# Optimization experiments

Measured on AMD Instinct MI355X. Metric: run time of the kernel, lower is better.

## Reference

```python
import jax, jax.numpy as jnp
from jax import lax
import numpy as np

B, T, I, H, O = 2048, 256, 88, 64, 13


def _lstm_layer(xs, w_ih, w_hh, b):
    # xs: [T, B, in], w_ih: [4H, in], w_hh: [4H, H], b: [4H] (b_ih + b_hh)
    Bb = xs.shape[1]
    Hh = w_hh.shape[1]

    def step(carry, x_t):
        h, c = carry
        g = x_t @ w_ih.T + h @ w_hh.T + b  # [B, 4H]
        i, f, gg, o = jnp.split(g, 4, axis=-1)  # PyTorch gate order: i, f, g, o
        i = jax.nn.sigmoid(i)
        f = jax.nn.sigmoid(f)
        gg = jnp.tanh(gg)
        o = jax.nn.sigmoid(o)
        c = f * c + i * gg
        h = o * jnp.tanh(c)
        return (h, c), h

    init = (jnp.zeros((Bb, Hh), xs.dtype), jnp.zeros((Bb, Hh), xs.dtype))
    (h_last, _), ys = lax.scan(step, init, xs)
    return ys, h_last


def setup_inputs() -> dict:
    key = jax.random.key(0)
    ks = jax.random.split(key, 12)
    s = lambda fan: 1.0 / np.sqrt(H)  # PyTorch LSTM init scale 1/sqrt(H)
    u = lambda k, shape: jax.random.uniform(k, shape, jnp.float32, -s(H), s(H))
    return {
        "x": jax.random.normal(ks[0], (B, T, I), jnp.float32),
        "w_ih0": u(ks[1], (4 * H, I)),
        "w_hh0": u(ks[2], (4 * H, H)),
        "b_ih0": u(ks[3], (4 * H,)),
        "b_hh0": u(ks[4], (4 * H,)),
        "w_ih1": u(ks[5], (4 * H, H)),
        "w_hh1": u(ks[6], (4 * H, H)),
        "b_ih1": u(ks[7], (4 * H,)),
        "b_hh1": u(ks[8], (4 * H,)),
        "fc_w": u(ks[9], (O, H)),
        "fc_b": u(ks[10], (O,)),
    }


def reference(x, w_ih0, w_hh0, b_ih0, b_hh0, w_ih1, w_hh1, b_ih1, b_hh1, fc_w, fc_b):
    xs = jnp.transpose(x, (1, 0, 2))  # [T, B, I]
    ys1, _ = _lstm_layer(xs, w_ih0, w_hh0, b_ih0 + b_hh0)  # [T, B, H]
    # inter-layer dropout and head dropout are identity in eval mode
    _, h_last = _lstm_layer(ys1, w_ih1, w_hh1, b_ih1 + b_hh1)  # [B, H]
    return h_last @ fc_w.T + fc_b  # [B, O]
```

## Files before the change

### kernel.cpp

```cpp
#include <hip/hip_runtime.h>
#include <hip/hip_bf16.h>


#define B_ 2048
#define T_ 256
#define I_ 88
#define H_ 64
#define O_ 13
#define NB 8
#define G4H 256

__device__ __align__(16) float g_ys1[(size_t)T_ * B_ * H_];
__device__ __align__(16) float g_wp[(I_ + H_ + H_ + H_) * G4H];

__device__ __forceinline__ float sigmoid_f(float v) {
    return 1.f / (1.f + __expf(-v));
}
__device__ __forceinline__ float tanh_f(float v) {
    return 1.f - 2.f / (__expf(2.f * v) + 1.f);
}

__global__ void prep_weights(const float* __restrict__ wih0, const float* __restrict__ whh0,
                             const float* __restrict__ wih1, const float* __restrict__ whh1) {
    int id = blockIdx.x * blockDim.x + threadIdx.x;
    const int S0 = I_ * G4H;
    const int S1 = S0 + H_ * G4H;
    const int S2 = S1 + H_ * G4H;
    const int S3 = S2 + H_ * G4H;
    if (id >= S3) return;
    const float* src;
    int base, K;
    if (id < S0)      { base = 0;  src = wih0; K = I_; }
    else if (id < S1) { base = S0; src = whh0; K = H_; }
    else if (id < S2) { base = S1; src = wih1; K = H_; }
    else              { base = S2; src = whh1; K = H_; }
    int loc = id - base;
    int k   = loc >> 8;
    int col = loc & 255;
    int hh  = col >> 2;
    int g   = col & 3;
    g_wp[id] = src[(g * H_ + hh) * K + k];
}

__global__ __launch_bounds__(256, 1) void lstm_l0(const float* __restrict__ x,
                                                  const float* __restrict__ bih,
                                                  const float* __restrict__ bhh) {
    extern __shared__ float sm[];
    float* w0  = sm;
    float* wh  = sm + I_ * G4H;
    float* hsh = sm + (I_ + H_) * G4H;

    const int tid = threadIdx.x;
    for (int i = tid; i < ((I_ + H_) * G4H) / 4; i += 256)
        ((float4*)sm)[i] = ((const float4*)g_wp)[i];
    for (int i = tid; i < NB * H_; i += 256) hsh[i] = 0.f;

    const int hh = tid & 63;
    const int rg = __builtin_amdgcn_readfirstlane(tid >> 6);
    const int row0 = blockIdx.x * NB + rg * 2;
    const float* xr0 = x + (size_t)row0 * (T_ * I_);
    const float* xr1 = xr0 + (T_ * I_);

    const float b0 = bih[hh] + bhh[hh];
    const float b1 = bih[64 + hh] + bhh[64 + hh];
    const float b2 = bih[128 + hh] + bhh[128 + hh];
    const float b3 = bih[192 + hh] + bhh[192 + hh];

    float c0 = 0.f, c1 = 0.f;
    float* ys0 = g_ys1 + (size_t)row0 * H_ + hh;

    __syncthreads();

    for (int t = 0; t < T_; ++t) {
        float a00 = b0, a01 = b1, a02 = b2, a03 = b3;
        float a10 = b0, a11 = b1, a12 = b2, a13 = b3;
        const float* xt0 = xr0 + t * I_;
        const float* xt1 = xr1 + t * I_;
#pragma unroll 8
        for (int k = 0; k < I_; ++k) {
            const float4 w = *(const float4*)&w0[(k << 8) + (hh << 2)];
            const float xv0 = xt0[k];
            const float xv1 = xt1[k];
            a00 += w.x * xv0; a01 += w.y * xv0; a02 += w.z * xv0; a03 += w.w * xv0;
            a10 += w.x * xv1; a11 += w.y * xv1; a12 += w.z * xv1; a13 += w.w * xv1;
        }
        const float* hc = hsh + (t & 1) * (NB * H_) + rg * 128;
#pragma unroll 8
        for (int k = 0; k < H_; ++k) {
            const float4 w = *(const float4*)&wh[(k << 8) + (hh << 2)];
            const float hv0 = hc[k];
            const float hv1 = hc[64 + k];
            a00 += w.x * hv0; a01 += w.y * hv0; a02 += w.z * hv0; a03 += w.w * hv0;
            a10 += w.x * hv1; a11 += w.y * hv1; a12 += w.z * hv1; a13 += w.w * hv1;
        }
        const float i0 = sigmoid_f(a00), f0 = sigmoid_f(a01), g0 = tanh_f(a02), o0 = sigmoid_f(a03);
        const float i1 = sigmoid_f(a10), f1 = sigmoid_f(a11), g1 = tanh_f(a12), o1 = sigmoid_f(a13);
        c0 = f0 * c0 + i0 * g0;
        c1 = f1 * c1 + i1 * g1;
        const float h0 = o0 * tanh_f(c0);
        const float h1 = o1 * tanh_f(c1);
        float* hn = hsh + ((t + 1) & 1) * (NB * H_) + rg * 128 + hh;
        hn[0]  = h0;
        hn[64] = h1;
        float* yb = ys0 + (size_t)t * (B_ * H_);
        yb[0]  = h0;
        yb[64] = h1;
        __syncthreads();
    }
}

__global__ __launch_bounds__(256, 1) void lstm_l1(const float* __restrict__ bih,
                                                  const float* __restrict__ bhh,
                                                  const float* __restrict__ fcw,
                                                  const float* __restrict__ fcb,
                                                  float* __restrict__ out) {
    extern __shared__ float sm[];
    float* wi  = sm;
    float* wh  = sm + H_ * G4H;
    float* hsh = sm + 2 * H_ * G4H;

    const int tid = threadIdx.x;
    const float* wp1 = g_wp + (I_ + H_) * G4H;
    for (int i = tid; i < (2 * H_ * G4H) / 4; i += 256)
        ((float4*)sm)[i] = ((const float4*)wp1)[i];
    for (int i = tid; i < NB * H_; i += 256) hsh[i] = 0.f;

    const int hh = tid & 63;
    const int rg = __builtin_amdgcn_readfirstlane(tid >> 6);
    const int row0 = blockIdx.x * NB + rg * 2;

    const float b0 = bih[hh] + bhh[hh];
    const float b1 = bih[64 + hh] + bhh[64 + hh];
    const float b2 = bih[128 + hh] + bhh[128 + hh];
    const float b3 = bih[192 + hh] + bhh[192 + hh];

    float c0 = 0.f, c1 = 0.f;
    const float* yr = g_ys1 + (size_t)row0 * H_;

    __syncthreads();

    for (int t = 0; t < T_; ++t) {
        float a00 = b0, a01 = b1, a02 = b2, a03 = b3;
        float a10 = b0, a11 = b1, a12 = b2, a13 = b3;
        const float* yt = yr + (size_t)t * (B_ * H_);
#pragma unroll 8
        for (int k = 0; k < H_; ++k) {
            const float4 w = *(const float4*)&wi[(k << 8) + (hh << 2)];
            const float yv0 = yt[k];
            const float yv1 = yt[64 + k];
            a00 += w.x * yv0; a01 += w.y * yv0; a02 += w.z * yv0; a03 += w.w * yv0;
            a10 += w.x * yv1; a11 += w.y * yv1; a12 += w.z * yv1; a13 += w.w * yv1;
        }
        const float* hc = hsh + (t & 1) * (NB * H_) + rg * 128;
#pragma unroll 8
        for (int k = 0; k < H_; ++k) {
            const float4 w = *(const float4*)&wh[(k << 8) + (hh << 2)];
            const float hv0 = hc[k];
            const float hv1 = hc[64 + k];
            a00 += w.x * hv0; a01 += w.y * hv0; a02 += w.z * hv0; a03 += w.w * hv0;
            a10 += w.x * hv1; a11 += w.y * hv1; a12 += w.z * hv1; a13 += w.w * hv1;
        }
        const float i0 = sigmoid_f(a00), f0 = sigmoid_f(a01), g0 = tanh_f(a02), o0 = sigmoid_f(a03);
        const float i1 = sigmoid_f(a10), f1 = sigmoid_f(a11), g1 = tanh_f(a12), o1 = sigmoid_f(a13);
        c0 = f0 * c0 + i0 * g0;
        c1 = f1 * c1 + i1 * g1;
        const float h0 = o0 * tanh_f(c0);
        const float h1 = o1 * tanh_f(c1);
        float* hn = hsh + ((t + 1) & 1) * (NB * H_) + rg * 128 + hh;
        hn[0]  = h0;
        hn[64] = h1;
        __syncthreads();
    }

    const float* hl = hsh;
    if (tid < NB * O_) {
        const int r = tid / O_;
        const int o = tid % O_;
        float s = fcb[o];
        const float* wrow = fcw + o * H_;
#pragma unroll 8
        for (int k = 0; k < H_; ++k) s += hl[r * H_ + k] * wrow[k];
        out[(size_t)(blockIdx.x * NB + r) * O_ + o] = s;
    }
}

extern "C" void kernel_launch(void* const* d_in, const int* in_sizes, int n_in,
                              void* d_out, int out_size, void* d_ws, size_t ws_size,
                              hipStream_t stream) {
    const float* x     = (const float*)d_in[0];
    const float* wih0  = (const float*)d_in[1];
    const float* whh0  = (const float*)d_in[2];
    const float* bih0  = (const float*)d_in[3];
    const float* bhh0  = (const float*)d_in[4];
    const float* wih1  = (const float*)d_in[5];
    const float* whh1  = (const float*)d_in[6];
    const float* bih1  = (const float*)d_in[7];
    const float* bhh1  = (const float*)d_in[8];
    const float* fcw   = (const float*)d_in[9];
    const float* fcb   = (const float*)d_in[10];
    float* out = (float*)d_out;

    const int lds0 = (I_ + H_) * G4H * 4 + 2 * NB * H_ * 4;
    const int lds1 = 2 * H_ * G4H * 4 + 2 * NB * H_ * 4;
    hipFuncSetAttribute((const void*)lstm_l0, hipFuncAttributeMaxDynamicSharedMemorySize, lds0);
    hipFuncSetAttribute((const void*)lstm_l1, hipFuncAttributeMaxDynamicSharedMemorySize, lds1);

    prep_weights<<<dim3(280), dim3(256), 0, stream>>>(wih0, whh0, wih1, whh1);
    lstm_l0<<<dim3(B_ / NB), dim3(256), lds0, stream>>>(x, bih0, bhh0);
    lstm_l1<<<dim3(B_ / NB), dim3(256), lds1, stream>>>(bih1, bhh1, fcw, fcb, out);
}
```

Before: 2.682 ms.

## Split LSTM into time-chunked input GEMMs and per-row recurrent kernels

Splits each layer's work into two parts. The input projection is computed as a batched GEMM over 32-step time chunks and stored as gate preactivations. A separate recurrent kernel then runs one block per batch row, keeping W_hh in registers, with h and c carried between chunk launches through global buffers. This removes the input matmul from the serial per-step loop, shrinks the layer-1 intermediate to a single chunk, and moves the recurrence to 2048 small blocks. In exchange it adds 32 kernel launches, global traffic for the preactivations, and two barriers per timestep with only one wave doing the cell update.

```diff
diff --git a/kernel.cpp b/kernel.cpp
--- a/kernel.cpp
+++ b/kernel.cpp
@@ -7,11 +7,16 @@
 #define I_ 88
 #define H_ 64
 #define O_ 13
-#define NB 8
 #define G4H 256
-
-__device__ __align__(16) float g_ys1[(size_t)T_ * B_ * H_];
-__device__ __align__(16) float g_wp[(I_ + H_ + H_ + H_) * G4H];
+#define TC 32
+#define CR (B_ * TC)
+#define NCK (T_ / TC)
+
+__device__ __align__(16) float g_gpre[(size_t)CR * G4H];
+__device__ __align__(16) float g_ysc[(size_t)CR * H_];
+__device__ __align__(16) float g_wp[(I_ + H_) * G4H];
+__device__ float g_h[2][B_ * H_];
+__device__ float g_c[2][B_ * H_];
 
 __device__ __forceinline__ float sigmoid_f(float v) {
     return 1.f / (1.f + __expf(-v));
@@ -20,20 +25,15 @@
     return 1.f - 2.f / (__expf(2.f * v) + 1.f);
 }
 
-__global__ void prep_weights(const float* __restrict__ wih0, const float* __restrict__ whh0,
-                             const float* __restrict__ wih1, const float* __restrict__ whh1) {
+__global__ void prep_weights(const float* __restrict__ wih0, const float* __restrict__ wih1) {
     int id = blockIdx.x * blockDim.x + threadIdx.x;
     const int S0 = I_ * G4H;
     const int S1 = S0 + H_ * G4H;
-    const int S2 = S1 + H_ * G4H;
-    const int S3 = S2 + H_ * G4H;
-    if (id >= S3) return;
+    if (id >= S1) return;
     const float* src;
     int base, K;
-    if (id < S0)      { base = 0;  src = wih0; K = I_; }
-    else if (id < S1) { base = S0; src = whh0; K = H_; }
-    else if (id < S2) { base = S1; src = wih1; K = H_; }
-    else              { base = S2; src = whh1; K = H_; }
+    if (id < S0) { base = 0;  src = wih0; K = I_; }
+    else         { base = S0; src = wih1; K = H_; }
     int loc = id - base;
     int k   = loc >> 8;
     int col = loc & 255;
@@ -42,170 +42,194 @@
     g_wp[id] = src[(g * H_ + hh) * K + k];
 }
 
-__global__ __launch_bounds__(256, 1) void lstm_l0(const float* __restrict__ x,
-                                                  const float* __restrict__ bih,
-                                                  const float* __restrict__ bhh) {
-    extern __shared__ float sm[];
-    float* w0  = sm;
-    float* wh  = sm + I_ * G4H;
-    float* hsh = sm + (I_ + H_) * G4H;
-
+__global__ __launch_bounds__(256, 1) void gemm_l0(const float* __restrict__ x, int ck) {
+    extern __shared__ __align__(16) float wl[];
     const int tid = threadIdx.x;
-    for (int i = tid; i < ((I_ + H_) * G4H) / 4; i += 256)
-        ((float4*)sm)[i] = ((const float4*)g_wp)[i];
-    for (int i = tid; i < NB * H_; i += 256) hsh[i] = 0.f;
-
-    const int hh = tid & 63;
-    const int rg = __builtin_amdgcn_readfirstlane(tid >> 6);
-    const int row0 = blockIdx.x * NB + rg * 2;
-    const float* xr0 = x + (size_t)row0 * (T_ * I_);
-    const float* xr1 = xr0 + (T_ * I_);
-
-    const float b0 = bih[hh] + bhh[hh];
-    const float b1 = bih[64 + hh] + bhh[64 + hh];
-    const float b2 = bih[128 + hh] + bhh[128 + hh];
-    const float b3 = bih[192 + hh] + bhh[192 + hh];
-
-    float c0 = 0.f, c1 = 0.f;
-    float* ys0 = g_ys1 + (size_t)row0 * H_ + hh;
-
+    for (int i = tid; i < (I_ * G4H) / 4; i += 256)
+        ((float4*)wl)[i] = ((const float4*)g_wp)[i];
     __syncthreads();
 
-    for (int t = 0; t < T_; ++t) {
-        float a00 = b0, a01 = b1, a02 = b2, a03 = b3;
-        float a10 = b0, a11 = b1, a12 = b2, a13 = b3;
-        const float* xt0 = xr0 + t * I_;
-        const float* xt1 = xr1 + t * I_;
-#pragma unroll 8
+    const int j  = tid & 63;
+    const int wv = __builtin_amdgcn_readfirstlane(tid >> 6);
+
+    for (int p = 0; p < 8; ++p) {
+        const int qb = (blockIdx.x << 8) + (p << 5) + (wv << 3);
+        const float* xr[8];
+#pragma unroll
+        for (int m = 0; m < 8; ++m) {
+            const int q = qb + m;
+            const long in_row = (long)(q & (B_ - 1)) * T_ + ck * TC + (q >> 11);
+            xr[m] = x + (size_t)in_row * I_;
+        }
+        float4 acc[8];
+#pragma unroll
+        for (int m = 0; m < 8; ++m) acc[m] = make_float4(0.f, 0.f, 0.f, 0.f);
+
+#pragma unroll 2
         for (int k = 0; k < I_; ++k) {
-            const float4 w = *(const float4*)&w0[(k << 8) + (hh << 2)];
-            const float xv0 = xt0[k];
-            const float xv1 = xt1[k];
-            a00 += w.x * xv0; a01 += w.y * xv0; a02 += w.z * xv0; a03 += w.w * xv0;
-            a10 += w.x * xv1; a11 += w.y * xv1; a12 += w.z * xv1; a13 += w.w * xv1;
-        }
-        const float* hc = hsh + (t & 1) * (NB * H_) + rg * 128;
-#pragma unroll 8
+            const float4 w4 = *(const float4*)&wl[(k << 8) + (j << 2)];
+#pragma unroll
+            for (int m = 0; m < 8; ++m) {
+                const float xv = xr[m][k];
+                acc[m].x += w4.x * xv; acc[m].y += w4.y * xv;
+                acc[m].z += w4.z * xv; acc[m].w += w4.w * xv;
+            }
+        }
+#pragma unroll
+        for (int m = 0; m < 8; ++m) {
+            float* o = g_gpre + (size_t)(qb + m) * G4H + j;
+            o[0]   = acc[m].x;
+            o[64]  = acc[m].y;
+            o[128] = acc[m].z;
+            o[192] = acc[m].w;
+        }
+    }
+}
+
+__global__ __launch_bounds__(256, 1) void gemm_l1() {
+    extern __shared__ __align__(16) float wl[];
+    const int tid = threadIdx.x;
+    for (int i = tid; i < (H_ * G4H) / 4; i += 256)
+        ((float4*)wl)[i] = ((const float4*)(g_wp + I_ * G4H))[i];
+    __syncthreads();
+
+    const int j  = tid & 63;
+    const int wv = __builtin_amdgcn_readfirstlane(tid >> 6);
+
+    for (int p = 0; p < 8; ++p) {
+        const int qb = (blockIdx.x << 8) + (p << 5) + (wv << 3);
+        const float* xr[8];
+#pragma unroll
+        for (int m = 0; m < 8; ++m) xr[m] = g_ysc + (size_t)(qb + m) * H_;
+
+        float4 acc[8];
+#pragma unroll
+        for (int m = 0; m < 8; ++m) acc[m] = make_float4(0.f, 0.f, 0.f, 0.f);
+
+#pragma unroll 2
         for (int k = 0; k < H_; ++k) {
-            const float4 w = *(const float4*)&wh[(k << 8) + (hh << 2)];
-            const float hv0 = hc[k];
-            const float hv1 = hc[64 + k];
-            a00 += w.x * hv0; a01 += w.y * hv0; a02 += w.z * hv0; a03 += w.w * hv0;
-            a10 += w.x * hv1; a11 += w.y * hv1; a12 += w.z * hv1; a13 += w.w * hv1;
-        }
-        const float i0 = sigmoid_f(a00), f0 = sigmoid_f(a01), g0 = tanh_f(a02), o0 = sigmoid_f(a03);
-        const float i1 = sigmoid_f(a10), f1 = sigmoid_f(a11), g1 = tanh_f(a12), o1 = sigmoid_f(a13);
-        c0 = f0 * c0 + i0 * g0;
-        c1 = f1 * c1 + i1 * g1;
-        const float h0 = o0 * tanh_f(c0);
-        const float h1 = o1 * tanh_f(c1);
-        float* hn = hsh + ((t + 1) & 1) * (NB * H_) + rg * 128 + hh;
-        hn[0]  = h0;
-        hn[64] = h1;
-        float* yb = ys0 + (size_t)t * (B_ * H_);
-        yb[0]  = h0;
-        yb[64] = h1;
+            const float4 w4 = *(const float4*)&wl[(k << 8) + (j << 2)];
+#pragma unroll
+            for (int m = 0; m < 8; ++m) {
+                const float xv = xr[m][k];
+                acc[m].x += w4.x * xv; acc[m].y += w4.y * xv;
+                acc[m].z += w4.z * xv; acc[m].w += w4.w * xv;
+            }
+        }
+#pragma unroll
+        for (int m = 0; m < 8; ++m) {
+            float* o = g_gpre + (size_t)(qb + m) * G4H + j;
+            o[0]   = acc[m].x;
+            o[64]  = acc[m].y;
+            o[128] = acc[m].z;
+            o[192] = acc[m].w;
+        }
+    }
+}
+
+__global__ __launch_bounds__(256, 1) void lstm_rec(const float* __restrict__ whh,
+                                                   const float* __restrict__ bih,
+                                                   const float* __restrict__ bhh,
+                                                   const int layer, const int ck,
+                                                   const float* __restrict__ fcw,
+                                                   const float* __restrict__ fcb,
+                                                   float* __restrict__ out) {
+    __shared__ __align__(16) float hl[H_];
+    __shared__ float xch[4][H_];
+
+    const int tid = threadIdx.x;
+    const int j   = tid & 63;
+    const int g   = __builtin_amdgcn_readfirstlane(tid >> 6);
+    const int r   = blockIdx.x;
+
+    float4 w[16];
+    const float* wrow = whh + (size_t)(g * H_ + j) * H_;
+#pragma unroll
+    for (int kk = 0; kk < 16; ++kk) w[kk] = ((const float4*)wrow)[kk];
+
+    const float bias = bih[g * H_ + j] + bhh[g * H_ + j];
+    if (tid < H_) hl[tid] = ck ? g_h[layer][r * H_ + tid] : 0.f;
+    float c = 0.f;
+    if (g == 0 && ck) c = g_c[layer][r * H_ + j];
+
+    const float* gp = g_gpre + (size_t)r * G4H + g * H_ + j;
+    float gpv = gp[0];
+    __syncthreads();
+
+    for (int tl = 0; tl < TC; ++tl) {
+        float a0 = 0.f, a1 = 0.f, a2 = 0.f, a3 = 0.f;
+#pragma unroll
+        for (int kk = 0; kk < 16; kk += 4) {
+            const float4 h0 = *(const float4*)&hl[(kk + 0) << 2];
+            a0 += w[kk + 0].x * h0.x; a0 += w[kk + 0].y * h0.y;
+            a0 += w[kk + 0].z * h0.z; a0 += w[kk + 0].w * h0.w;
+            const float4 h1 = *(const float4*)&hl[(kk + 1) << 2];
+            a1 += w[kk + 1].x * h1.x; a1 += w[kk + 1].y * h1.y;
+            a1 += w[kk + 1].z * h1.z; a1 += w[kk + 1].w * h1.w;
+            const float4 h2 = *(const float4*)&hl[(kk + 2) << 2];
+            a2 += w[kk + 2].x * h2.x; a2 += w[kk + 2].y * h2.y;
+            a2 += w[kk + 2].z * h2.z; a2 += w[kk + 2].w * h2.w;
+            const float4 h3 = *(const float4*)&hl[(kk + 3) << 2];
+            a3 += w[kk + 3].x * h3.x; a3 += w[kk + 3].y * h3.y;
+            a3 += w[kk + 3].z * h3.z; a3 += w[kk + 3].w * h3.w;
+        }
+        const float pre = bias + gpv + ((a0 + a1) + (a2 + a3));
+        if (tl + 1 < TC) gpv = gp[(size_t)(tl + 1) * B_ * G4H];
+
+        const float act = (g == 2) ? tanh_f(pre) : sigmoid_f(pre);
+        xch[g][j] = act;
         __syncthreads();
-    }
-}
-
-__global__ __launch_bounds__(256, 1) void lstm_l1(const float* __restrict__ bih,
-                                                  const float* __restrict__ bhh,
-                                                  const float* __restrict__ fcw,
-                                                  const float* __restrict__ fcb,
-                                                  float* __restrict__ out) {
-    extern __shared__ float sm[];
-    float* wi  = sm;
-    float* wh  = sm + H_ * G4H;
-    float* hsh = sm + 2 * H_ * G4H;
-
-    const int tid = threadIdx.x;
-    const float* wp1 = g_wp + (I_ + H_) * G4H;
-    for (int i = tid; i < (2 * H_ * G4H) / 4; i += 256)
-        ((float4*)sm)[i] = ((const float4*)wp1)[i];
-    for (int i = tid; i < NB * H_; i += 256) hsh[i] = 0.f;
-
-    const int hh = tid & 63;
-    const int rg = __builtin_amdgcn_readfirstlane(tid >> 6);
-    const int row0 = blockIdx.x * NB + rg * 2;
-
-    const float b0 = bih[hh] + bhh[hh];
-    const float b1 = bih[64 + hh] + bhh[64 + hh];
-    const float b2 = bih[128 + hh] + bhh[128 + hh];
-    const float b3 = bih[192 + hh] + bhh[192 + hh];
-
-    float c0 = 0.f, c1 = 0.f;
-    const float* yr = g_ys1 + (size_t)row0 * H_;
-
-    __syncthreads();
-
-    for (int t = 0; t < T_; ++t) {
-        float a00 = b0, a01 = b1, a02 = b2, a03 = b3;
-        float a10 = b0, a11 = b1, a12 = b2, a13 = b3;
-        const float* yt = yr + (size_t)t * (B_ * H_);
-#pragma unroll 8
-        for (int k = 0; k < H_; ++k) {
-            const float4 w = *(const float4*)&wi[(k << 8) + (hh << 2)];
-            const float yv0 = yt[k];
-            const float yv1 = yt[64 + k];
-            a00 += w.x * yv0; a01 += w.y * yv0; a02 += w.z * yv0; a03 += w.w * yv0;
-            a10 += w.x * yv1; a11 += w.y * yv1; a12 += w.z * yv1; a13 += w.w * yv1;
-        }
-        const float* hc = hsh + (t & 1) * (NB * H_) + rg * 128;
-#pragma unroll 8
-        for (int k = 0; k < H_; ++k) {
-            const float4 w = *(const float4*)&wh[(k << 8) + (hh << 2)];
-            const float hv0 = hc[k];
-            const float hv1 = hc[64 + k];
-            a00 += w.x * hv0; a01 += w.y * hv0; a02 += w.z * hv0; a03 += w.w * hv0;
-            a10 += w.x * hv1; a11 += w.y * hv1; a12 += w.z * hv1; a13 += w.w * hv1;
-        }
-        const float i0 = sigmoid_f(a00), f0 = sigmoid_f(a01), g0 = tanh_f(a02), o0 = sigmoid_f(a03);
-        const float i1 = sigmoid_f(a10), f1 = sigmoid_f(a11), g1 = tanh_f(a12), o1 = sigmoid_f(a13);
-        c0 = f0 * c0 + i0 * g0;
-        c1 = f1 * c1 + i1 * g1;
-        const float h0 = o0 * tanh_f(c0);
-        const float h1 = o1 * tanh_f(c1);
-        float* hn = hsh + ((t + 1) & 1) * (NB * H_) + rg * 128 + hh;
-        hn[0]  = h0;
-        hn[64] = h1;
+
+        if (g == 0) {
+            const float iv = xch[0][j], fv = xch[1][j], gv = xch[2][j], ov = xch[3][j];
+            c = fv * c + iv * gv;
+            const float h = ov * tanh_f(c);
+            hl[j] = h;
+            if (layer == 0) g_ysc[((size_t)tl * B_ + r) * H_ + j] = h;
+        }
         __syncthreads();
     }
 
-    const float* hl = hsh;
-    if (tid < NB * O_) {
-        const int r = tid / O_;
-        const int o = tid % O_;
-        float s = fcb[o];
-        const float* wrow = fcw + o * H_;
-#pragma unroll 8
-        for (int k = 0; k < H_; ++k) s += hl[r * H_ + k] * wrow[k];
-        out[(size_t)(blockIdx.x * NB + r) * O_ + o] = s;
+    if (g == 0) {
+        g_h[layer][r * H_ + j] = hl[j];
+        g_c[layer][r * H_ + j] = c;
+        if (layer == 1 && ck == NCK - 1 && j < O_) {
+            float s = fcb[j];
+            const float* wr = fcw + j * H_;
+#pragma unroll
+            for (int k = 0; k < H_; ++k) s += hl[k] * wr[k];
+            out[(size_t)r * O_ + j] = s;
+        }
     }
 }
 
 extern "C" void kernel_launch(void* const* d_in, const int* in_sizes, int n_in,
                               void* d_out, int out_size, void* d_ws, size_t ws_size,
                               hipStream_t stream) {
-    const float* x     = (const float*)d_in[0];
-    const float* wih0  = (const float*)d_in[1];
-    const float* whh0  = (const float*)d_in[2];
-    const float* bih0  = (const float*)d_in[3];
-    const float* bhh0  = (const float*)d_in[4];
-    const float* wih1  = (const float*)d_in[5];
-    const float* whh1  = (const float*)d_in[6];
-    const float* bih1  = (const float*)d_in[7];
-    const float* bhh1  = (const float*)d_in[8];
-    const float* fcw   = (const float*)d_in[9];
-    const float* fcb   = (const float*)d_in[10];
+    const float* x    = (const float*)d_in[0];
+    const float* wih0 = (const float*)d_in[1];
+    const float* whh0 = (const float*)d_in[2];
+    const float* bih0 = (const float*)d_in[3];
+    const float* bhh0 = (const float*)d_in[4];
+    const float* wih1 = (const float*)d_in[5];
+    const float* whh1 = (const float*)d_in[6];
+    const float* bih1 = (const float*)d_in[7];
+    const float* bhh1 = (const float*)d_in[8];
+    const float* fcw  = (const float*)d_in[9];
+    const float* fcb  = (const float*)d_in[10];
     float* out = (float*)d_out;
 
-    const int lds0 = (I_ + H_) * G4H * 4 + 2 * NB * H_ * 4;
-    const int lds1 = 2 * H_ * G4H * 4 + 2 * NB * H_ * 4;
-    hipFuncSetAttribute((const void*)lstm_l0, hipFuncAttributeMaxDynamicSharedMemorySize, lds0);
-    hipFuncSetAttribute((const void*)lstm_l1, hipFuncAttributeMaxDynamicSharedMemorySize, lds1);
-
-    prep_weights<<<dim3(280), dim3(256), 0, stream>>>(wih0, whh0, wih1, whh1);
-    lstm_l0<<<dim3(B_ / NB), dim3(256), lds0, stream>>>(x, bih0, bhh0);
-    lstm_l1<<<dim3(B_ / NB), dim3(256), lds1, stream>>>(bih1, bhh1, fcw, fcb, out);
-}
+    const int lds0 = I_ * G4H * 4;
+    const int lds1 = H_ * G4H * 4;
+    hipFuncSetAttribute((const void*)gemm_l0, hipFuncAttributeMaxDynamicSharedMemorySize, lds0);
+    hipFuncSetAttribute((const void*)gemm_l1, hipFuncAttributeMaxDynamicSharedMemorySize, lds1);
+
+    prep_weights<<<dim3(152), dim3(256), 0, stream>>>(wih0, wih1);
+
+    for (int ck = 0; ck < NCK; ++ck) {
+        gemm_l0<<<dim3(CR / 256), dim3(256), lds0, stream>>>(x, ck);
+        lstm_rec<<<dim3(B_), dim3(256), 0, stream>>>(whh0, bih0, bhh0, 0, ck, fcw, fcb, out);
+        gemm_l1<<<dim3(CR / 256), dim3(256), lds1, stream>>>();
+        lstm_rec<<<dim3(B_), dim3(256), 0, stream>>>(whh1, bih1, bhh1, 1, ck, fcw, fcb, out);
+    }
+}
```

New measurement: 2.453 ms. 1.09x faster.
